# Optimization experiments

Hardware: AMD Instinct MI355X
Metric: run time of the kernel (lower is better)

## Reference

```python
import jax, jax.numpy as jnp
import numpy as np

B, C_IN, N = 64, 64, 4097          # N = T + 1 (index 0 is the null node)
T = N - 1
HID, LAT = 128, 64
EPS = 1e-5


def _tree_conv(trees, children, W, b):
    # trees: (B, C, N); children: (B, 3T) int indices into node axis
    Bn, C, _ = trees.shape
    idx = jnp.broadcast_to(children[:, None, :], (Bn, C, children.shape[1]))
    g = jnp.take_along_axis(trees, idx, axis=2)        # (B, C, 3T) gather
    g = g.reshape(Bn, C, -1, 3)                        # (B, C, T, 3)
    out = jnp.einsum('bctk,ock->bot', g, W) + b[None, :, None]  # (B, O, T)
    zero = jnp.zeros((Bn, out.shape[1], 1), out.dtype)  # null-node column
    return jnp.concatenate([zero, out], axis=2)         # (B, O, T+1)


def _tree_layer_norm(x):
    # normalize over (channels, nodes) per example; torch.std -> ddof=1
    mean = jnp.mean(x, axis=(1, 2), keepdims=True)
    std = jnp.std(x, axis=(1, 2), ddof=1, keepdims=True)
    return (x - mean) / (std + EPS)


def _encode(feats, children, W1, b1, W2, b2):
    x = _tree_conv(feats, children, W1, b1)
    x = jax.nn.relu(_tree_layer_norm(x))
    x = _tree_conv(x, children, W2, b2)
    x = jax.nn.relu(_tree_layer_norm(x))   # dropout is identity in eval
    return jnp.max(x, axis=2)              # DynamicPooling: (B, HID)


def setup_inputs() -> dict:
    key = jax.random.key(0)
    ks = jax.random.split(key, 12)
    s_in = 1.0 / np.sqrt(3 * C_IN)
    s_h = 1.0 / np.sqrt(3 * HID)
    s_fc = 1.0 / np.sqrt(2 * HID)
    return {
        'logical_feats': jax.random.normal(ks[0], (B, C_IN, N), jnp.float32),
        'physical_feats': jax.random.normal(ks[1], (B, C_IN, N), jnp.float32),
        'children': jax.random.randint(ks[2], (B, 3 * T), 0, N, jnp.int32),
        'Wl1': jax.random.normal(ks[3], (HID, C_IN, 3), jnp.float32) * s_in,
        'bl1': jnp.zeros((HID,), jnp.float32),
        'Wl2': jax.random.normal(ks[4], (HID, HID, 3), jnp.float32) * s_h,
        'bl2': jnp.zeros((HID,), jnp.float32),
        'Wp1': jax.random.normal(ks[5], (HID, C_IN, 3), jnp.float32) * s_in,
        'bp1': jnp.zeros((HID,), jnp.float32),
        'Wp2': jax.random.normal(ks[6], (HID, HID, 3), jnp.float32) * s_h,
        'bp2': jnp.zeros((HID,), jnp.float32),
        'Wmu': jax.random.normal(ks[7], (LAT, 2 * HID), jnp.float32) * s_fc,
        'bmu': jnp.zeros((LAT,), jnp.float32),
        'Wlv': jax.random.normal(ks[8], (LAT, 2 * HID), jnp.float32) * s_fc,
        'blv': jnp.zeros((LAT,), jnp.float32),
    }


def reference(logical_feats, physical_feats, children,
              Wl1, bl1, Wl2, bl2, Wp1, bp1, Wp2, bp2,
              Wmu, bmu, Wlv, blv):
    # NOTE: source module passes log_children to BOTH encoders; kept faithful.
    l_embed = _encode(logical_feats, children, Wl1, bl1, Wl2, bl2)
    p_embed = _encode(physical_feats, children, Wp1, bp1, Wp2, bp2)
    combined = jnp.concatenate([l_embed, p_embed], axis=-1)  # (B, 2*HID)
    mu = combined @ Wmu.T + bmu
    logvar = combined @ Wlv.T + blv
    return mu, logvar
```

## Files before the change

### kernel.cpp

```cpp
#include <hip/hip_runtime.h>
#include <hip/hip_bf16.h>

#define NODES 4097
#define TT 4096
#define CIN 64
#define HID 128
#define BATCH 64
#define EPS 1e-5f

typedef short bf16x8 __attribute__((ext_vector_type(8)));
typedef float f32x16 __attribute__((ext_vector_type(16)));

__device__ __forceinline__ void load_lds16(const void* g, void* l) {
    __builtin_amdgcn_global_load_lds(
        (const __attribute__((address_space(1))) unsigned int*)(uintptr_t)g,
        (__attribute__((address_space(3))) unsigned int*)(uintptr_t)l,
        16, 0, 0);
}

__global__ __launch_bounds__(256) void k_transpose(const float* __restrict__ f0,
                                                   const float* __restrict__ f1,
                                                   __hip_bfloat16* __restrict__ out) {
    __shared__ float tile[32][33];
    int z = blockIdx.z;
    int enc = z >> 6, b = z & 63;
    const float* in = enc ? f1 : f0;
    __hip_bfloat16* o = out + (size_t)enc * BATCH * NODES * CIN;
    int n0 = blockIdx.x * 32;
    int c0 = blockIdx.y * 32;
    int tx = threadIdx.x, ty = threadIdx.y;
    for (int i = 0; i < 32; i += 8) {
        int n = n0 + tx, c = c0 + ty + i;
        float v = 0.f;
        if (n < NODES) v = in[((size_t)b * CIN + c) * NODES + n];
        tile[ty + i][tx] = v;
    }
    __syncthreads();
    for (int i = 0; i < 32; i += 8) {
        int n = n0 + ty + i, c = c0 + tx;
        if (n < NODES) o[((size_t)b * NODES + n) * CIN + c] = __float2bfloat16(tile[tx][ty + i]);
    }
}

__global__ void k_wprep(const float* __restrict__ W0, const float* __restrict__ W1,
                        __hip_bfloat16* __restrict__ Wp, int C) {
    int enc = blockIdx.y;
    const float* W = enc ? W1 : W0;
    __hip_bfloat16* o = Wp + (size_t)enc * 3 * C * HID;
    int id = blockIdx.x * 256 + threadIdx.x;
    int total = 3 * C * HID / 8;
    if (id >= total) return;
    int lane = id & 63;
    int ct = (id >> 6) & 3;
    int ks = id >> 8;
    int n = ct * 32 + (lane & 31);
    int kb = ks * 16 + (lane >> 5) * 8;
    union { int4 i; __hip_bfloat16 h[8]; } u;
#pragma unroll
    for (int j = 0; j < 8; ++j) {
        int k = kb + j;
        int slot = k / C, c = k % C;
        u.h[j] = __float2bfloat16(W[(n * C + c) * 3 + slot]);
    }
    ((int4*)o)[id] = u.i;
}

template <int C, bool POOL>
__global__ __launch_bounds__(256) void k_conv_mfma(
    const __hip_bfloat16* __restrict__ xT,
    const int* __restrict__ children,
    const __hip_bfloat16* __restrict__ Wp,
    const float* __restrict__ bias0, const float* __restrict__ bias1,
    __hip_bfloat16* __restrict__ y,
    float* __restrict__ sums,
    float* __restrict__ pool_part) {
    constexpr int KSc = C / 16;
    constexpr int TOTK = 3 * KSc;
    constexpr int NPH = (C == 64) ? 1 : 3;
    constexpr int PK = TOTK / NPH;
    const int b = blockIdx.y;
    const int enc = blockIdx.z;
    const int t0 = blockIdx.x * 128;
    const int tid = threadIdx.x;
    const int lane = tid & 63;
    const int w = tid >> 6;
    const int rg2 = w >> 1, ct2 = w & 1;

    __shared__ __align__(16) char A_lds[4 * PK * 1024];

    const __hip_bfloat16* x = xT + (size_t)enc * BATCH * NODES * C;
    const int4* WpB = (const int4*)(Wp + (size_t)enc * 3 * C * HID);
    const float* bias = enc ? bias1 : bias0;
    const int sb = enc * BATCH + b;

    f32x16 acc[2][2] = {};
    const size_t rowbase = (size_t)b * NODES;
    const long cb3 = (long)b * (3 * TT);
    const int tnode = t0 + w * 32 + (lane & 31);

    for (int ph = 0; ph < NPH; ++ph) {
        if (ph) __syncthreads();
#pragma unroll
        for (int kk = 0; kk < PK; ++kk) {
            int ksg = ph * PK + kk;
            int slot = ksg / KSc, ksl = ksg % KSc;
            int child = children[cb3 + (long)tnode * 3 + slot];
            const char* g = (const char*)(x + (rowbase + child) * C)
                          + ksl * 32 + (lane >> 5) * 16;
            load_lds16(g, A_lds + (w * PK + kk) * 1024);
        }
        __syncthreads();
#pragma unroll
        for (int kk = 0; kk < PK; ++kk) {
            int ksg = ph * PK + kk;
            bf16x8 a0 = *(const bf16x8*)(A_lds + ((2 * rg2 + 0) * PK + kk) * 1024 + lane * 16);
            bf16x8 a1 = *(const bf16x8*)(A_lds + ((2 * rg2 + 1) * PK + kk) * 1024 + lane * 16);
            union { int4 i; bf16x8 v; } b0, b1;
            b0.i = WpB[(ksg * 4 + 2 * ct2 + 0) * 64 + lane];
            b1.i = WpB[(ksg * 4 + 2 * ct2 + 1) * 64 + lane];
            acc[0][0] = __builtin_amdgcn_mfma_f32_32x32x16_bf16(a0, b0.v, acc[0][0], 0, 0, 0);
            acc[0][1] = __builtin_amdgcn_mfma_f32_32x32x16_bf16(a0, b1.v, acc[0][1], 0, 0, 0);
            acc[1][0] = __builtin_amdgcn_mfma_f32_32x32x16_bf16(a1, b0.v, acc[1][0], 0, 0, 0);
            acc[1][1] = __builtin_amdgcn_mfma_f32_32x32x16_bf16(a1, b1.v, acc[1][1], 0, 0, 0);
        }
    }

    float bsum = 0.f, bss = 0.f;
    float lmax[2] = {-3.4e38f, -3.4e38f};
    __hip_bfloat16* yp = POOL ? nullptr : (y + (size_t)enc * BATCH * NODES * HID);
#pragma unroll
    for (int rgi = 0; rgi < 2; ++rgi) {
#pragma unroll
        for (int cti = 0; cti < 2; ++cti) {
            int o = 64 * ct2 + 32 * cti + (lane & 31);
            float bv = bias[o];
            int rbase = t0 + 64 * rg2 + 32 * rgi + 4 * (lane >> 5) + 1;
            f32x16 a = acc[rgi][cti];
#pragma unroll
            for (int reg = 0; reg < 16; ++reg) {
                float v = a[reg] + bv;
                bsum += v;
                bss += v * v;
                if (POOL) {
                    lmax[cti] = fmaxf(lmax[cti], v);
                } else {
                    int row = rbase + (reg & 3) + 8 * (reg >> 2);
                    yp[(rowbase + row) * HID + o] = __float2bfloat16(v);
                }
            }
        }
    }
    if (!POOL && blockIdx.x == 0 && tid < HID)
        yp[rowbase * HID + tid] = __float2bfloat16(0.f);

    __syncthreads();
    float* red = (float*)A_lds;
    float* pm = red + 512;
    red[tid] = bsum;
    red[256 + tid] = bss;
    if (POOL) {
        int slice = 2 * rg2 + (lane >> 5);
        pm[(64 * ct2 + (lane & 31)) * 4 + slice] = lmax[0];
        pm[(64 * ct2 + 32 + (lane & 31)) * 4 + slice] = lmax[1];
    }
    __syncthreads();
    for (int s = 128; s > 0; s >>= 1) {
        if (tid < s) { red[tid] += red[tid + s]; red[256 + tid] += red[256 + tid + s]; }
        __syncthreads();
    }
    if (tid == 0) {
        atomicAdd(&sums[sb * 2], red[0]);
        atomicAdd(&sums[sb * 2 + 1], red[256]);
    }
    if (POOL && tid < HID) {
        float m = fmaxf(fmaxf(pm[tid * 4], pm[tid * 4 + 1]),
                        fmaxf(pm[tid * 4 + 2], pm[tid * 4 + 3]));
        pool_part[((size_t)sb * 32 + blockIdx.x) * HID + tid] = m;
    }
}

__global__ void k_stats(const float* __restrict__ sums, float* __restrict__ ms) {
    int s = threadIdx.x;
    const float M = (float)HID * (float)NODES;
    float S = sums[s * 2], SS = sums[s * 2 + 1];
    float mean = S / M;
    float var = (SS - S * S / M) / (M - 1.f);
    float sd = sqrtf(fmaxf(var, 0.f));
    ms[s * 2] = mean;
    ms[s * 2 + 1] = 1.f / (sd + EPS);
}

__global__ __launch_bounds__(256) void k_norm(__hip_bfloat16* __restrict__ y,
                                              const float* __restrict__ ms) {
    constexpr int Q = NODES * HID / 8;
    int s = blockIdx.y;
    int q = blockIdx.x * 256 + threadIdx.x;
    if (q >= Q) return;
    float mean = ms[s * 2], scale = ms[s * 2 + 1];
    int4* p = (int4*)(y + (size_t)s * NODES * HID) + q;
    union { int4 i; __hip_bfloat16 h[8]; } u;
    u.i = *p;
#pragma unroll
    for (int j = 0; j < 8; ++j) {
        float f = (__bfloat162float(u.h[j]) - mean) * scale;
        u.h[j] = __float2bfloat16(f > 0.f ? f : 0.f);
    }
    *p = u.i;
}

__global__ __launch_bounds__(128) void k_pool_fin(const float* __restrict__ part,
                                                  const float* __restrict__ ms1,
                                                  float* __restrict__ combined) {
    int b = blockIdx.x, enc = blockIdx.y, o = threadIdx.x;
    int sb = enc * BATCH + b;
    float m = 0.f;
#pragma unroll 4
    for (int s = 0; s < 32; ++s)
        m = fmaxf(m, part[((size_t)sb * 32 + s) * HID + o]);
    float v = (m - ms1[sb * 2]) * ms1[sb * 2 + 1];
    combined[b * 256 + enc * 128 + o] = v > 0.f ? v : 0.f;
}

__global__ __launch_bounds__(128) void k_fc(const float* __restrict__ combined,
                                            const float* __restrict__ Wmu, const float* __restrict__ bmu,
                                            const float* __restrict__ Wlv, const float* __restrict__ blv,
                                            float* __restrict__ out) {
    int b = blockIdx.x;
    int tid = threadIdx.x;
    __shared__ float cb[256];
    cb[tid] = combined[b * 256 + tid];
    cb[tid + 128] = combined[b * 256 + tid + 128];
    __syncthreads();
    const float* W = (tid < 64) ? Wmu : Wlv;
    int l = tid & 63;
    float s = (tid < 64) ? bmu[l] : blv[l];
    for (int j = 0; j < 256; ++j) s += cb[j] * W[l * 256 + j];
    out[(tid < 64 ? 0 : BATCH * 64) + b * 64 + l] = s;
}

extern "C" void kernel_launch(void* const* d_in, const int* in_sizes, int n_in,
                              void* d_out, int out_size, void* d_ws, size_t ws_size,
                              hipStream_t stream) {
    const int* children = (const int*)d_in[2];
    const float* Wmu = (const float*)d_in[11];
    const float* bmu = (const float*)d_in[12];
    const float* Wlv = (const float*)d_in[13];
    const float* blv = (const float*)d_in[14];

    char* ws = (char*)d_ws;
    size_t off = 0;
    auto alloc = [&](size_t bytes) { void* p = ws + off; off += (bytes + 255) & ~(size_t)255; return p; };
    float* sums = (float*)alloc(2 * 2 * BATCH * 2 * sizeof(float));
    float* msbuf = (float*)alloc(2 * 2 * BATCH * 2 * sizeof(float));
    float* combined = (float*)alloc((size_t)BATCH * 256 * sizeof(float));
    float* pool_part = (float*)alloc((size_t)2 * BATCH * 32 * HID * sizeof(float));
    __hip_bfloat16* Wp1 = (__hip_bfloat16*)alloc((size_t)2 * 3 * CIN * HID * sizeof(__hip_bfloat16));
    __hip_bfloat16* Wp2 = (__hip_bfloat16*)alloc((size_t)2 * 3 * HID * HID * sizeof(__hip_bfloat16));
    __hip_bfloat16* fT = (__hip_bfloat16*)alloc((size_t)2 * BATCH * NODES * CIN * sizeof(__hip_bfloat16));
    __hip_bfloat16* y1 = (__hip_bfloat16*)alloc((size_t)2 * BATCH * NODES * HID * sizeof(__hip_bfloat16));

    hipMemsetAsync(sums, 0, 2 * 2 * BATCH * 2 * sizeof(float), stream);

    k_wprep<<<dim3(3 * CIN * HID / 8 / 256, 2), 256, 0, stream>>>(
        (const float*)d_in[3], (const float*)d_in[7], Wp1, CIN);
    k_wprep<<<dim3(3 * HID * HID / 8 / 256, 2), 256, 0, stream>>>(
        (const float*)d_in[5], (const float*)d_in[9], Wp2, HID);
    k_transpose<<<dim3(129, 2, 2 * BATCH), dim3(32, 8), 0, stream>>>(
        (const float*)d_in[0], (const float*)d_in[1], fT);

    k_conv_mfma<CIN, false><<<dim3(TT / 128, BATCH, 2), 256, 0, stream>>>(
        fT, children, Wp1, (const float*)d_in[4], (const float*)d_in[8], y1, sums, nullptr);
    k_stats<<<1, 128, 0, stream>>>(sums, msbuf);
    k_norm<<<dim3((NODES * HID / 8 + 255) / 256, 2 * BATCH), 256, 0, stream>>>(y1, msbuf);
    k_conv_mfma<HID, true><<<dim3(TT / 128, BATCH, 2), 256, 0, stream>>>(
        y1, children, Wp2, (const float*)d_in[6], (const float*)d_in[10], nullptr,
        sums + 256, pool_part);
    k_stats<<<1, 128, 0, stream>>>(sums + 256, msbuf + 256);
    k_pool_fin<<<dim3(BATCH, 2), 128, 0, stream>>>(pool_part, msbuf + 256, combined);

    k_fc<<<BATCH, 128, 0, stream>>>(combined, Wmu, bmu, Wlv, blv, (float*)d_out);
}
```

Measured before the change: 438.6 us.

## Remap conv blocks XCD-aware per batch, halve row tile, hoist child lookups

The conv kernels now run on a flat grid of 8192 blocks. Each block handles 64 nodes instead of 128, and block IDs are swizzled so every block of a given batch example lands on the same XCD. The aim is to keep each example's gathered node rows resident in that XCD's L2. The three child indices per node are read once into row pointers instead of being re-read per k-slice. The first layer is split into two load phases to match the smaller LDS tile. In exchange, each block reuses the weight fragments over fewer rows, and the stats atomics and pool partials double.

```diff
diff --git a/kernel.cpp b/kernel.cpp
--- a/kernel.cpp
+++ b/kernel.cpp
@@ -65,7 +65,7 @@
     ((int4*)o)[id] = u.i;
 }
 
-template <int C, bool POOL>
+template <int C, int NPH, bool POOL>
 __global__ __launch_bounds__(256) void k_conv_mfma(
     const __hip_bfloat16* __restrict__ xT,
     const int* __restrict__ children,
@@ -76,52 +76,60 @@
     float* __restrict__ pool_part) {
     constexpr int KSc = C / 16;
     constexpr int TOTK = 3 * KSc;
-    constexpr int NPH = (C == 64) ? 1 : 3;
     constexpr int PK = TOTK / NPH;
-    const int b = blockIdx.y;
-    const int enc = blockIdx.z;
-    const int t0 = blockIdx.x * 128;
+    int L = blockIdx.x;
+    int xcd = L & 7;
+    int idx = L >> 3;
+    int xt = idx & 63;
+    int bg = (idx >> 6) & 7;
+    int enc = idx >> 9;
+    int b = xcd + 8 * bg;
+    const int t0 = xt * 64;
     const int tid = threadIdx.x;
     const int lane = tid & 63;
     const int w = tid >> 6;
     const int rg2 = w >> 1, ct2 = w & 1;
 
-    __shared__ __align__(16) char A_lds[4 * PK * 1024];
+    __shared__ __align__(16) char A_lds[2 * PK * 1024];
 
     const __hip_bfloat16* x = xT + (size_t)enc * BATCH * NODES * C;
     const int4* WpB = (const int4*)(Wp + (size_t)enc * 3 * C * HID);
     const float* bias = enc ? bias1 : bias0;
     const int sb = enc * BATCH + b;
 
-    f32x16 acc[2][2] = {};
     const size_t rowbase = (size_t)b * NODES;
     const long cb3 = (long)b * (3 * TT);
-    const int tnode = t0 + w * 32 + (lane & 31);
-
+    const int tnode = t0 + rg2 * 32 + (lane & 31);
+
+    const char* rowp[3];
+#pragma unroll
+    for (int s = 0; s < 3; ++s) {
+        int child = children[cb3 + (long)tnode * 3 + s];
+        rowp[s] = (const char*)(x + (rowbase + child) * C) + (lane >> 5) * 16;
+    }
+
+    f32x16 acc[2] = {};
+
+#pragma unroll
     for (int ph = 0; ph < NPH; ++ph) {
         if (ph) __syncthreads();
 #pragma unroll
+        for (int i = 0; i < PK / 2; ++i) {
+            int kk = (w & 1) * (PK / 2) + i;
+            int ksg = ph * PK + kk;
+            int slot = ksg / KSc, ksl = ksg % KSc;
+            load_lds16(rowp[slot] + ksl * 32, A_lds + (rg2 * PK + kk) * 1024);
+        }
+        __syncthreads();
+#pragma unroll
         for (int kk = 0; kk < PK; ++kk) {
             int ksg = ph * PK + kk;
-            int slot = ksg / KSc, ksl = ksg % KSc;
-            int child = children[cb3 + (long)tnode * 3 + slot];
-            const char* g = (const char*)(x + (rowbase + child) * C)
-                          + ksl * 32 + (lane >> 5) * 16;
-            load_lds16(g, A_lds + (w * PK + kk) * 1024);
-        }
-        __syncthreads();
-#pragma unroll
-        for (int kk = 0; kk < PK; ++kk) {
-            int ksg = ph * PK + kk;
-            bf16x8 a0 = *(const bf16x8*)(A_lds + ((2 * rg2 + 0) * PK + kk) * 1024 + lane * 16);
-            bf16x8 a1 = *(const bf16x8*)(A_lds + ((2 * rg2 + 1) * PK + kk) * 1024 + lane * 16);
+            bf16x8 a = *(const bf16x8*)(A_lds + (rg2 * PK + kk) * 1024 + lane * 16);
             union { int4 i; bf16x8 v; } b0, b1;
             b0.i = WpB[(ksg * 4 + 2 * ct2 + 0) * 64 + lane];
             b1.i = WpB[(ksg * 4 + 2 * ct2 + 1) * 64 + lane];
-            acc[0][0] = __builtin_amdgcn_mfma_f32_32x32x16_bf16(a0, b0.v, acc[0][0], 0, 0, 0);
-            acc[0][1] = __builtin_amdgcn_mfma_f32_32x32x16_bf16(a0, b1.v, acc[0][1], 0, 0, 0);
-            acc[1][0] = __builtin_amdgcn_mfma_f32_32x32x16_bf16(a1, b0.v, acc[1][0], 0, 0, 0);
-            acc[1][1] = __builtin_amdgcn_mfma_f32_32x32x16_bf16(a1, b1.v, acc[1][1], 0, 0, 0);
+            acc[0] = __builtin_amdgcn_mfma_f32_32x32x16_bf16(a, b0.v, acc[0], 0, 0, 0);
+            acc[1] = __builtin_amdgcn_mfma_f32_32x32x16_bf16(a, b1.v, acc[1], 0, 0, 0);
         }
     }
 
@@ -129,28 +137,25 @@
     float lmax[2] = {-3.4e38f, -3.4e38f};
     __hip_bfloat16* yp = POOL ? nullptr : (y + (size_t)enc * BATCH * NODES * HID);
 #pragma unroll
-    for (int rgi = 0; rgi < 2; ++rgi) {
-#pragma unroll
-        for (int cti = 0; cti < 2; ++cti) {
-            int o = 64 * ct2 + 32 * cti + (lane & 31);
-            float bv = bias[o];
-            int rbase = t0 + 64 * rg2 + 32 * rgi + 4 * (lane >> 5) + 1;
-            f32x16 a = acc[rgi][cti];
-#pragma unroll
-            for (int reg = 0; reg < 16; ++reg) {
-                float v = a[reg] + bv;
-                bsum += v;
-                bss += v * v;
-                if (POOL) {
-                    lmax[cti] = fmaxf(lmax[cti], v);
-                } else {
-                    int row = rbase + (reg & 3) + 8 * (reg >> 2);
-                    yp[(rowbase + row) * HID + o] = __float2bfloat16(v);
-                }
+    for (int cti = 0; cti < 2; ++cti) {
+        int o = 64 * ct2 + 32 * cti + (lane & 31);
+        float bv = bias[o];
+        int rbase = t0 + 32 * rg2 + 4 * (lane >> 5) + 1;
+        f32x16 a = acc[cti];
+#pragma unroll
+        for (int reg = 0; reg < 16; ++reg) {
+            float v = a[reg] + bv;
+            bsum += v;
+            bss += v * v;
+            if (POOL) {
+                lmax[cti] = fmaxf(lmax[cti], v);
+            } else {
+                int row = rbase + (reg & 3) + 8 * (reg >> 2);
+                yp[(rowbase + row) * HID + o] = __float2bfloat16(v);
             }
         }
     }
-    if (!POOL && blockIdx.x == 0 && tid < HID)
+    if (!POOL && xt == 0 && tid < HID)
         yp[rowbase * HID + tid] = __float2bfloat16(0.f);
 
     __syncthreads();
@@ -164,8 +169,8 @@
         pm[(64 * ct2 + 32 + (lane & 31)) * 4 + slice] = lmax[1];
     }
     __syncthreads();
-    for (int s = 128; s > 0; s >>= 1) {
-        if (tid < s) { red[tid] += red[tid + s]; red[256 + tid] += red[256 + tid + s]; }
+    for (int s2 = 128; s2 > 0; s2 >>= 1) {
+        if (tid < s2) { red[tid] += red[tid + s2]; red[256 + tid] += red[256 + tid + s2]; }
         __syncthreads();
     }
     if (tid == 0) {
@@ -175,7 +180,7 @@
     if (POOL && tid < HID) {
         float m = fmaxf(fmaxf(pm[tid * 4], pm[tid * 4 + 1]),
                         fmaxf(pm[tid * 4 + 2], pm[tid * 4 + 3]));
-        pool_part[((size_t)sb * 32 + blockIdx.x) * HID + tid] = m;
+        pool_part[((size_t)sb * 64 + xt) * HID + tid] = m;
     }
 }
 
@@ -215,8 +220,8 @@
     int sb = enc * BATCH + b;
     float m = 0.f;
 #pragma unroll 4
-    for (int s = 0; s < 32; ++s)
-        m = fmaxf(m, part[((size_t)sb * 32 + s) * HID + o]);
+    for (int s = 0; s < 64; ++s)
+        m = fmaxf(m, part[((size_t)sb * 64 + s) * HID + o]);
     float v = (m - ms1[sb * 2]) * ms1[sb * 2 + 1];
     combined[b * 256 + enc * 128 + o] = v > 0.f ? v : 0.f;
 }
@@ -253,7 +258,7 @@
     float* sums = (float*)alloc(2 * 2 * BATCH * 2 * sizeof(float));
     float* msbuf = (float*)alloc(2 * 2 * BATCH * 2 * sizeof(float));
     float* combined = (float*)alloc((size_t)BATCH * 256 * sizeof(float));
-    float* pool_part = (float*)alloc((size_t)2 * BATCH * 32 * HID * sizeof(float));
+    float* pool_part = (float*)alloc((size_t)2 * BATCH * 64 * HID * sizeof(float));
     __hip_bfloat16* Wp1 = (__hip_bfloat16*)alloc((size_t)2 * 3 * CIN * HID * sizeof(__hip_bfloat16));
     __hip_bfloat16* Wp2 = (__hip_bfloat16*)alloc((size_t)2 * 3 * HID * HID * sizeof(__hip_bfloat16));
     __hip_bfloat16* fT = (__hip_bfloat16*)alloc((size_t)2 * BATCH * NODES * CIN * sizeof(__hip_bfloat16));
@@ -268,11 +273,11 @@
     k_transpose<<<dim3(129, 2, 2 * BATCH), dim3(32, 8), 0, stream>>>(
         (const float*)d_in[0], (const float*)d_in[1], fT);
 
-    k_conv_mfma<CIN, false><<<dim3(TT / 128, BATCH, 2), 256, 0, stream>>>(
+    k_conv_mfma<CIN, 2, false><<<8192, 256, 0, stream>>>(
         fT, children, Wp1, (const float*)d_in[4], (const float*)d_in[8], y1, sums, nullptr);
     k_stats<<<1, 128, 0, stream>>>(sums, msbuf);
     k_norm<<<dim3((NODES * HID / 8 + 255) / 256, 2 * BATCH), 256, 0, stream>>>(y1, msbuf);
-    k_conv_mfma<HID, true><<<dim3(TT / 128, BATCH, 2), 256, 0, stream>>>(
+    k_conv_mfma<HID, 3, true><<<8192, 256, 0, stream>>>(
         y1, children, Wp2, (const float*)d_in[6], (const float*)d_in[10], nullptr,
         sums + 256, pool_part);
     k_stats<<<1, 128, 0, stream>>>(sums + 256, msbuf + 256);
```

After: 486.1 us. 1.11x slower.
